# Performance work log

Measured on AMD Instinct MI355X. Metric: run time of the kernel, lower is better.

Reference implementation:

```python
import jax, jax.numpy as jnp
import numpy as np

LIMIT_A = -0.1
LIMIT_B = 1.1
MASK_INIT_MEAN = float(np.log(1 - 0.2) - np.log(0.2))  # droprate_init = 0.2

B, T, I, H = 64, 512, 1024, 1024


def _hard_concrete_gate(mask_logits):
    # deterministic (eval) gate: hardtanh(sigmoid(mask) * (limit_b - limit_a) + limit_a, 0, 1)
    return jnp.clip(jax.nn.sigmoid(mask_logits) * (LIMIT_B - LIMIT_A) + LIMIT_A, 0.0, 1.0)


def setup_inputs() -> dict:
    key = jax.random.key(0)
    ks = jax.random.split(key, 9)
    xavier = float(np.sqrt(6.0 / (H + I)))
    seq = jax.random.normal(ks[0], (B, T, I), dtype=jnp.float32)
    w_ih = jax.random.uniform(ks[1], (H, I), jnp.float32, -xavier, xavier)
    w_hh = jax.random.uniform(ks[2], (H, H), jnp.float32, -xavier, xavier)
    b_ih = jnp.zeros((H,), jnp.float32)
    b_hh = jnp.zeros((H,), jnp.float32)
    # mask logits ~ N(log((1-droprate)/droprate), 0.01)
    w_ih_mask = MASK_INIT_MEAN + 0.01 * jax.random.normal(ks[3], (H, I), jnp.float32)
    w_hh_mask = MASK_INIT_MEAN + 0.01 * jax.random.normal(ks[4], (H, H), jnp.float32)
    b_ih_mask = MASK_INIT_MEAN + 0.01 * jax.random.normal(ks[5], (H,), jnp.float32)
    b_hh_mask = MASK_INIT_MEAN + 0.01 * jax.random.normal(ks[6], (H,), jnp.float32)
    return {
        "seq": seq,
        "w_ih": w_ih, "w_ih_mask": w_ih_mask,
        "w_hh": w_hh, "w_hh_mask": w_hh_mask,
        "b_ih": b_ih, "b_ih_mask": b_ih_mask,
        "b_hh": b_hh, "b_hh_mask": b_hh_mask,
    }


def reference(seq, w_ih, w_ih_mask, w_hh, w_hh_mask, b_ih, b_ih_mask, b_hh, b_hh_mask):
    # gated (L0 hard-concrete, deterministic) weights
    W_ih = _hard_concrete_gate(w_ih_mask) * w_ih  # [H, I]
    W_hh = _hard_concrete_gate(w_hh_mask) * w_hh  # [H, H]
    B_ih = _hard_concrete_gate(b_ih_mask) * b_ih  # [H]
    B_hh = _hard_concrete_gate(b_hh_mask) * b_hh  # [H]

    # precompute input projection for all timesteps: [B, T, H]
    x_proj = jnp.einsum('bti,hi->bth', seq, W_ih) + B_ih + B_hh

    h0 = jnp.zeros((seq.shape[0], W_hh.shape[0]), seq.dtype)

    def step(h, xp_t):  # xp_t: [B, H]
        h_new = jnp.tanh(xp_t + h @ W_hh.T)
        return h_new, h_new

    h_last, hs = jax.lax.scan(step, h0, jnp.swapaxes(x_proj, 0, 1))  # hs: [T, B, H]
    output = jnp.swapaxes(hs, 0, 1)  # [B, T, H] (batch_first)
    return output, h_last[None]  # hidden: [num_layers*num_dirs, B, H]
```

## Files before the change

### kernel.cpp

```cpp
#include <hip/hip_runtime.h>
#include <cmath>


typedef _Float16 v8h __attribute__((ext_vector_type(8)));
typedef float    v4f __attribute__((ext_vector_type(4)));
typedef unsigned long long u64;

#define BB 64
#define TT 512
#define HH 1024
#define OUT_MAIN (BB * TT * HH)
#define OFF_WIH  0u
#define OFF_WHH  (2u << 20)
#define OFF_BIAS (4u << 20)
#define OFF_HBUF ((4u << 20) + 8192u)
#define OFF_FLG  ((4u << 20) + 8192u + 262144u)

#define ALD(p)    __hip_atomic_load((p),        __ATOMIC_RELAXED, __HIP_MEMORY_SCOPE_AGENT)
#define AST(p, v) __hip_atomic_store((p), (v),  __ATOMIC_RELAXED, __HIP_MEMORY_SCOPE_AGENT)

__device__ __forceinline__ float hc_gate(float x) {
    float s = 1.0f / (1.0f + __expf(-x));
    float g = s * 1.2f - 0.1f;
    return fminf(1.0f, fmaxf(0.0f, g));
}

__device__ __forceinline__ float fast_tanh(float x) {
    float e = __expf(2.0f * x);
    return 1.0f - 2.0f * __builtin_amdgcn_rcpf(e + 1.0f);
}

__global__ void prep_kernel(const float* __restrict__ w_ih, const float* __restrict__ w_ih_mask,
                            const float* __restrict__ w_hh, const float* __restrict__ w_hh_mask,
                            const float* __restrict__ b_ih, const float* __restrict__ b_ih_mask,
                            const float* __restrict__ b_hh, const float* __restrict__ b_hh_mask,
                            _Float16* __restrict__ Wih, _Float16* __restrict__ Whh,
                            float* __restrict__ bias, _Float16* __restrict__ hbuf,
                            int* __restrict__ flg) {
    const int idx = blockIdx.x * 256 + threadIdx.x;
    Wih[idx] = (_Float16)(hc_gate(w_ih_mask[idx]) * w_ih[idx]);
    Whh[idx] = (_Float16)(hc_gate(w_hh_mask[idx]) * w_hh[idx]);
    if (idx < HH)
        bias[idx] = hc_gate(b_ih_mask[idx]) * b_ih[idx] + hc_gate(b_hh_mask[idx]) * b_hh[idx];
    if (idx < 131072) hbuf[idx] = (_Float16)0.0f;
    if (idx < 32) flg[idx] = 0;
}

__global__ __launch_bounds__(256, 2) void gemm_xproj(const float* __restrict__ seq,
                                                     const _Float16* __restrict__ Wih,
                                                     const float* __restrict__ bias,
                                                     float* __restrict__ out) {
    __shared__ _Float16 As[128][40];
    __shared__ _Float16 Bs[128][40];

    const int tid  = threadIdx.x;
    const int lane = tid & 63;
    const int w    = tid >> 6;
    const int bid  = blockIdx.x;
    const int m0 = (bid >> 3) * 128;
    const int n0 = (bid & 7) * 128;
    const int mw = (w >> 1) * 64, nw = (w & 1) * 64;

    const int sr = tid >> 1;
    const int sc = (tid & 1) * 16;

    const float*    aSrc = seq + (m0 + sr) * HH + sc;
    const _Float16* bSrc = Wih + (n0 + sr) * HH + sc;

    const v4f vzero = {0.f, 0.f, 0.f, 0.f};
    v4f acc[4][4];
#pragma unroll
    for (int i = 0; i < 4; i++)
#pragma unroll
        for (int j = 0; j < 4; j++) acc[i][j] = vzero;

    const int arow = mw + (lane & 15);
    const int brow = nw + (lane & 15);
    const int kq   = (lane >> 4) * 8;

    for (int k0 = 0; k0 < HH; k0 += 32) {
        float4 f0 = *(const float4*)(aSrc + 0);
        float4 f1 = *(const float4*)(aSrc + 4);
        float4 f2 = *(const float4*)(aSrc + 8);
        float4 f3 = *(const float4*)(aSrc + 12);
        v8h a0 = {(_Float16)f0.x, (_Float16)f0.y, (_Float16)f0.z, (_Float16)f0.w,
                  (_Float16)f1.x, (_Float16)f1.y, (_Float16)f1.z, (_Float16)f1.w};
        v8h a1 = {(_Float16)f2.x, (_Float16)f2.y, (_Float16)f2.z, (_Float16)f2.w,
                  (_Float16)f3.x, (_Float16)f3.y, (_Float16)f3.z, (_Float16)f3.w};
        v8h b0 = *(const v8h*)(bSrc + 0);
        v8h b1 = *(const v8h*)(bSrc + 8);
        *(v8h*)&As[sr][sc]     = a0;
        *(v8h*)&As[sr][sc + 8] = a1;
        *(v8h*)&Bs[sr][sc]     = b0;
        *(v8h*)&Bs[sr][sc + 8] = b1;
        __syncthreads();

        v8h af[4], bf[4];
#pragma unroll
        for (int mi = 0; mi < 4; mi++) af[mi] = *(const v8h*)&As[mi * 16 + arow][kq];
#pragma unroll
        for (int ni = 0; ni < 4; ni++) bf[ni] = *(const v8h*)&Bs[ni * 16 + brow][kq];
#pragma unroll
        for (int mi = 0; mi < 4; mi++)
#pragma unroll
            for (int ni = 0; ni < 4; ni++)
                acc[mi][ni] = __builtin_amdgcn_mfma_f32_16x16x32_f16(af[mi], bf[ni], acc[mi][ni], 0, 0, 0);
        __syncthreads();
        aSrc += 32;
        bSrc += 32;
    }

    const int colb = lane & 15;
    const int rowq = (lane >> 4) * 4;
#pragma unroll
    for (int ni = 0; ni < 4; ni++) {
        const int col = n0 + nw + ni * 16 + colb;
        const float bz = bias[col];
#pragma unroll
        for (int mi = 0; mi < 4; mi++) {
            const int row = m0 + mw + mi * 16 + rowq;
#pragma unroll
            for (int r = 0; r < 4; r++)
                out[(row + r) * HH + col] = acc[mi][ni][r] + bz;
        }
    }
}

__global__ __launch_bounds__(256, 1) void rnn_steps(const _Float16* __restrict__ Whh,
                                                    float* __restrict__ out,
                                                    _Float16* __restrict__ hbuf,
                                                    int* __restrict__ flg) {
    __shared__ _Float16 tile[16 * 128];
    __shared__ __align__(16) u64 hlds[32 * 128];

    const int tid  = threadIdx.x;
    const int lane = tid & 63;
    const int w    = tid >> 6;
    const int bid  = blockIdx.x;
    const int g    = bid >> 3;
    const int jw   = bid & 7;

    const int l15 = lane & 15;
    const int kq  = (lane >> 4) * 8;
    const int bq  = (lane >> 4) * 4;

    const int col0 = jw * 128 + w * 32 + l15;

    v8h Wf[64];
    {
        const _Float16* w0 = Whh + col0 * 1024 + kq;
        const _Float16* w1 = Whh + (col0 + 16) * 1024 + kq;
#pragma unroll
        for (int c = 0; c < 32; c++) {
            Wf[c * 2 + 0] = *(const v8h*)(w0 + c * 32);
            Wf[c * 2 + 1] = *(const v8h*)(w1 + c * 32);
        }
    }

    {
        u64* q = &hlds[(jw * 4 + w) * 128 + lane * 2];
        q[0] = 0ull; q[1] = 0ull;
    }

    float xp[2][4];
#pragma unroll
    for (int r = 0; r < 4; r++) {
        const float* xs = out + ((g * 16 + bq + r) * TT + 0) * HH + col0;
        xp[0][r] = xs[0];
        xp[1][r] = xs[16];
    }

    int* fg = flg + g * 8;

    for (int t = 0; t < TT; t++) {
        if (tid == 0) {
            for (;;) {
                int m = ALD(fg + 0);
#pragma unroll
                for (int i = 1; i < 8; i++) {
                    int v = ALD(fg + i);
                    m = v < m ? v : m;
                }
                if (m >= t) break;
                __builtin_amdgcn_s_sleep(1);
            }
        }
        __syncthreads();

        {
            const u64* hbp = (const u64*)(hbuf + ((t & 1) * 4 + g) * 16384);
            u64 dv[16];
#pragma unroll
            for (int i = 0; i < 8; i++) {
                if (i != jw) {
                    const u64* p = hbp + (i * 4 + w) * 128 + lane * 2;
                    dv[2 * i]     = ALD(p);
                    dv[2 * i + 1] = ALD(p + 1);
                }
            }
#pragma unroll
            for (int i = 0; i < 8; i++) {
                if (i != jw) {
                    u64* q = &hlds[(i * 4 + w) * 128 + lane * 2];
                    q[0] = dv[2 * i];
                    q[1] = dv[2 * i + 1];
                }
            }
        }
        __syncthreads();

        v4f aA0 = {0.f, 0.f, 0.f, 0.f}, aA1 = aA0, aB0 = aA0, aB1 = aA0;
#pragma unroll
        for (int cc = 0; cc < 8; cc++) {
            const u64* q = &hlds[cc * 512 + lane * 2];
            v8h h0 = *(const v8h*)(q);
            v8h h1 = *(const v8h*)(q + 128);
            v8h h2 = *(const v8h*)(q + 256);
            v8h h3 = *(const v8h*)(q + 384);
            aA0 = __builtin_amdgcn_mfma_f32_16x16x32_f16(h0, Wf[(cc * 4 + 0) * 2 + 0], aA0, 0, 0, 0);
            aA1 = __builtin_amdgcn_mfma_f32_16x16x32_f16(h0, Wf[(cc * 4 + 0) * 2 + 1], aA1, 0, 0, 0);
            aB0 = __builtin_amdgcn_mfma_f32_16x16x32_f16(h1, Wf[(cc * 4 + 1) * 2 + 0], aB0, 0, 0, 0);
            aB1 = __builtin_amdgcn_mfma_f32_16x16x32_f16(h1, Wf[(cc * 4 + 1) * 2 + 1], aB1, 0, 0, 0);
            aA0 = __builtin_amdgcn_mfma_f32_16x16x32_f16(h2, Wf[(cc * 4 + 2) * 2 + 0], aA0, 0, 0, 0);
            aA1 = __builtin_amdgcn_mfma_f32_16x16x32_f16(h2, Wf[(cc * 4 + 2) * 2 + 1], aA1, 0, 0, 0);
            aB0 = __builtin_amdgcn_mfma_f32_16x16x32_f16(h3, Wf[(cc * 4 + 3) * 2 + 0], aB0, 0, 0, 0);
            aB1 = __builtin_amdgcn_mfma_f32_16x16x32_f16(h3, Wf[(cc * 4 + 3) * 2 + 1], aB1, 0, 0, 0);
        }
        const v4f av0 = aA0 + aB0;
        const v4f av1 = aA1 + aB1;

        float hv[2][4];
#pragma unroll
        for (int r = 0; r < 4; r++) {
            hv[0][r] = fast_tanh(xp[0][r] + av0[r]);
            hv[1][r] = fast_tanh(xp[1][r] + av1[r]);
            const int row = bq + r;
            const int sw  = (row & 7) << 4;
            char* base = (char*)tile + row * 256;
            *(_Float16*)(base + (((w * 32 + l15) * 2) ^ sw))      = (_Float16)hv[0][r];
            *(_Float16*)(base + (((w * 32 + 16 + l15) * 2) ^ sw)) = (_Float16)hv[1][r];
        }
        __syncthreads();

        {
            const int cpr = tid >> 6;
            const int l   = tid & 63;
            const int row = l & 15;
            const int cb  = (cpr * 32 + (l >> 4) * 8) * 2;
            union { v8h v; u64 u[2]; } uu;
            uu.v = *(const v8h*)((const char*)tile + row * 256 + (cb ^ ((row & 7) << 4)));
            u64* dst = (u64*)(hbuf + (((t + 1) & 1) * 4 + g) * 16384 + (jw * 4 + cpr) * 512) + l * 2;
            AST(dst,     uu.u[0]);
            AST(dst + 1, uu.u[1]);
            u64* q = &hlds[(jw * 4 + cpr) * 128 + l * 2];
            q[0] = uu.u[0];
            q[1] = uu.u[1];
        }
        __syncthreads();

        if (tid == 0) AST(&fg[jw], t + 1);

#pragma unroll
        for (int r = 0; r < 4; r++) {
            const int bg = g * 16 + bq + r;
            float* o = out + (bg * TT + t) * HH + col0;
            o[0]  = hv[0][r];
            o[16] = hv[1][r];
            if (t == TT - 1) {
                float* o2 = out + OUT_MAIN + bg * HH + col0;
                o2[0]  = hv[0][r];
                o2[16] = hv[1][r];
            }
        }
        if (t + 1 < TT) {
#pragma unroll
            for (int r = 0; r < 4; r++) {
                const float* xs = out + ((g * 16 + bq + r) * TT + (t + 1)) * HH + col0;
                xp[0][r] = xs[0];
                xp[1][r] = xs[16];
            }
        }
    }
}

extern "C" void kernel_launch(void* const* d_in, const int* in_sizes, int n_in,
                              void* d_out, int out_size, void* d_ws, size_t ws_size,
                              hipStream_t stream) {
    const float* seq       = (const float*)d_in[0];
    const float* w_ih      = (const float*)d_in[1];
    const float* w_ih_mask = (const float*)d_in[2];
    const float* w_hh      = (const float*)d_in[3];
    const float* w_hh_mask = (const float*)d_in[4];
    const float* b_ih      = (const float*)d_in[5];
    const float* b_ih_mask = (const float*)d_in[6];
    const float* b_hh      = (const float*)d_in[7];
    const float* b_hh_mask = (const float*)d_in[8];

    float* out = (float*)d_out;
    char*  ws  = (char*)d_ws;
    _Float16* Wih  = (_Float16*)(ws + OFF_WIH);
    _Float16* Whh  = (_Float16*)(ws + OFF_WHH);
    float*    bias = (float*)(ws + OFF_BIAS);
    _Float16* hbuf = (_Float16*)(ws + OFF_HBUF);
    int*      flg  = (int*)(ws + OFF_FLG);

    prep_kernel<<<dim3(4096), dim3(256), 0, stream>>>(w_ih, w_ih_mask, w_hh, w_hh_mask,
                                                      b_ih, b_ih_mask, b_hh, b_hh_mask,
                                                      Wih, Whh, bias, hbuf, flg);
    gemm_xproj<<<dim3(2048), dim3(256), 0, stream>>>(seq, Wih, bias, out);
    rnn_steps<<<dim3(32), dim3(256), 0, stream>>>(Whh, out, hbuf, flg);
}
```

Baseline: 2.404 ms.

## Replace block-level flag barrier with per-wave sequence flags and wave polling

Swaps the single per-block step flag, which was polled by thread 0 and followed by __syncthreads, for per-wave sequence counters in a double-buffered flag array. Each wave polls only the 7 peer waves whose hidden-state slice it consumes and publishes its own slice with its own flag after a vmcnt wait. This removes two block-wide barriers per timestep from the serial recurrence critical path. The cost is more flag traffic and fragile memory ordering, since relaxed atomics plus s_waitcnt stand in for release/acquire semantics.

```diff
diff --git a/kernel.cpp b/kernel.cpp
--- a/kernel.cpp
+++ b/kernel.cpp
@@ -14,7 +14,7 @@
 #define OFF_WHH  (2u << 20)
 #define OFF_BIAS (4u << 20)
 #define OFF_HBUF ((4u << 20) + 8192u)
-#define OFF_FLG  ((4u << 20) + 8192u + 262144u)
+#define OFF_SEQ  ((4u << 20) + 8192u + 262144u)
 
 #define ALD(p)    __hip_atomic_load((p),        __ATOMIC_RELAXED, __HIP_MEMORY_SCOPE_AGENT)
 #define AST(p, v) __hip_atomic_store((p), (v),  __ATOMIC_RELAXED, __HIP_MEMORY_SCOPE_AGENT)
@@ -36,14 +36,14 @@
                             const float* __restrict__ b_hh, const float* __restrict__ b_hh_mask,
                             _Float16* __restrict__ Wih, _Float16* __restrict__ Whh,
                             float* __restrict__ bias, _Float16* __restrict__ hbuf,
-                            int* __restrict__ flg) {
+                            int* __restrict__ seqf) {
     const int idx = blockIdx.x * 256 + threadIdx.x;
     Wih[idx] = (_Float16)(hc_gate(w_ih_mask[idx]) * w_ih[idx]);
     Whh[idx] = (_Float16)(hc_gate(w_hh_mask[idx]) * w_hh[idx]);
     if (idx < HH)
         bias[idx] = hc_gate(b_ih_mask[idx]) * b_ih[idx] + hc_gate(b_hh_mask[idx]) * b_hh[idx];
     if (idx < 131072) hbuf[idx] = (_Float16)0.0f;
-    if (idx < 32) flg[idx] = 0;
+    if (idx < 256) seqf[idx] = 0;
 }
 
 __global__ __launch_bounds__(256, 2) void gemm_xproj(const float* __restrict__ seq,
@@ -129,7 +129,7 @@
 __global__ __launch_bounds__(256, 1) void rnn_steps(const _Float16* __restrict__ Whh,
                                                     float* __restrict__ out,
                                                     _Float16* __restrict__ hbuf,
-                                                    int* __restrict__ flg) {
+                                                    int* __restrict__ seqf) {
     __shared__ _Float16 tile[16 * 128];
     __shared__ __align__(16) u64 hlds[32 * 128];
 
@@ -170,22 +170,18 @@
         xp[1][r] = xs[16];
     }
 
-    int* fg = flg + g * 8;
+    const int pollIdx = (lane < 8 && lane != jw) ? (lane * 4 + w) : -1;
 
     for (int t = 0; t < TT; t++) {
-        if (tid == 0) {
-            for (;;) {
-                int m = ALD(fg + 0);
-#pragma unroll
-                for (int i = 1; i < 8; i++) {
-                    int v = ALD(fg + i);
-                    m = v < m ? v : m;
-                }
-                if (m >= t) break;
-                __builtin_amdgcn_s_sleep(1);
-            }
-        }
-        __syncthreads();
+        int* sqp = seqf + ((t & 1) * 4 + g) * 32;
+
+        for (;;) {
+            int ok = 1;
+            if (pollIdx >= 0) ok = (ALD(sqp + pollIdx) >= t) ? 1 : 0;
+            if (__all(ok)) break;
+            __builtin_amdgcn_s_sleep(1);
+        }
+        asm volatile("" ::: "memory");
 
         {
             const u64* hbp = (const u64*)(hbuf + ((t & 1) * 4 + g) * 16384);
@@ -243,22 +239,20 @@
         __syncthreads();
 
         {
-            const int cpr = tid >> 6;
-            const int l   = tid & 63;
-            const int row = l & 15;
-            const int cb  = (cpr * 32 + (l >> 4) * 8) * 2;
+            const int row = lane & 15;
+            const int cb  = (w * 32 + (lane >> 4) * 8) * 2;
             union { v8h v; u64 u[2]; } uu;
             uu.v = *(const v8h*)((const char*)tile + row * 256 + (cb ^ ((row & 7) << 4)));
-            u64* dst = (u64*)(hbuf + (((t + 1) & 1) * 4 + g) * 16384 + (jw * 4 + cpr) * 512) + l * 2;
+            u64* dst = (u64*)(hbuf + (((t + 1) & 1) * 4 + g) * 16384) + (jw * 4 + w) * 128 + lane * 2;
             AST(dst,     uu.u[0]);
             AST(dst + 1, uu.u[1]);
-            u64* q = &hlds[(jw * 4 + cpr) * 128 + l * 2];
+            u64* q = &hlds[(jw * 4 + w) * 128 + lane * 2];
             q[0] = uu.u[0];
             q[1] = uu.u[1];
         }
-        __syncthreads();
-
-        if (tid == 0) AST(&fg[jw], t + 1);
+        asm volatile("s_waitcnt vmcnt(0)" ::: "memory");
+        if (lane == 0)
+            AST(seqf + (((t + 1) & 1) * 4 + g) * 32 + jw * 4 + w, t + 1);
 
 #pragma unroll
         for (int r = 0; r < 4; r++) {
@@ -302,11 +296,11 @@
     _Float16* Whh  = (_Float16*)(ws + OFF_WHH);
     float*    bias = (float*)(ws + OFF_BIAS);
     _Float16* hbuf = (_Float16*)(ws + OFF_HBUF);
-    int*      flg  = (int*)(ws + OFF_FLG);
+    int*      seqf = (int*)(ws + OFF_SEQ);
 
     prep_kernel<<<dim3(4096), dim3(256), 0, stream>>>(w_ih, w_ih_mask, w_hh, w_hh_mask,
                                                       b_ih, b_ih_mask, b_hh, b_hh_mask,
-                                                      Wih, Whh, bias, hbuf, flg);
+                                                      Wih, Whh, bias, hbuf, seqf);
     gemm_xproj<<<dim3(2048), dim3(256), 0, stream>>>(seq, Wih, bias, out);
-    rnn_steps<<<dim3(32), dim3(256), 0, stream>>>(Whh, out, hbuf, flg);
-}
+    rnn_steps<<<dim3(32), dim3(256), 0, stream>>>(Whh, out, hbuf, seqf);
+}
```

Result: faster. 2.320 ms (-3.5%).
